# Kernel tuning notes

Measured on AMD Instinct MI355X. Metric: run time of the kernel, lower is better.

The kernel has to match this reference:

```python
import jax, jax.numpy as jnp
import numpy as np


def setup_inputs() -> dict:
    key = jax.random.key(0)
    k1, k2, k3 = jax.random.split(key, 3)
    B, A, C = 32, 16384, 81
    pred_logits = jax.random.normal(k1, (B, A, C), dtype=jnp.float32)
    target = jax.random.uniform(k2, (B, A, C), dtype=jnp.float32)
    depth = jax.random.randint(k3, (B, A, 1), 0, 3, dtype=jnp.int32)
    return {"pred_logits": pred_logits, "target": target, "depth": depth,
            "negpos_ratio": 3}


def reference(pred_logits, target, depth, negpos_ratio):
    B, A, C = pred_logits.shape
    # BCE-with-logits, elementwise (stable): softplus(x) - t*x
    ce = jax.nn.softplus(pred_logits) - target * pred_logits        # [B,A,C]
    max_ce = jnp.max(ce, axis=2)                                    # [B,A]
    depth_v = depth.reshape(B, A)
    # zero out rows already matched (positives) so they never rank as negatives
    max_ce = jnp.where(depth_v != 0, jnp.zeros((), ce.dtype), max_ce)
    # double-argsort rank trick: rank of each anchor in descending max_ce order
    order = jnp.argsort(-max_ce, axis=1)                            # [B,A]
    idx_rank = jnp.argsort(order, axis=1)                           # [B,A]
    num_pos = jnp.sum(depth_v > 0, axis=1)                          # [B]
    num_neg = jnp.minimum(negpos_ratio * num_pos, A - 1)            # [B]
    neg = idx_rank < num_neg[:, None]                               # [B,A] bool
    mask = (depth_v > 0) | neg                                      # [B,A] bool
    return ce * mask[:, :, None].astype(ce.dtype)                   # [B,A,C]
```

## Files before the change

kernel.cpp:

```cpp
#include <hip/hip_runtime.h>
#include <cstdint>
#include <cstddef>

#define NUM_C 81
#define NUM_A 16384
#define A_TILE 128
#define TILE_ELEMS (A_TILE * NUM_C)
#define TILE_F4    (TILE_ELEMS / 4)

__device__ __forceinline__ float ce_one(float x, float t) {
    float sp = fmaxf(x, 0.f) + __logf(1.f + __expf(-fabsf(x)));
    return fmaf(-t, x, sp);
}

__global__ __launch_bounds__(256)
void ce_max_tile(const float* __restrict__ logits,
                 const float* __restrict__ target,
                 const int* __restrict__ depth,
                 float* __restrict__ out,
                 float* __restrict__ max_ce,
                 int n_anchors) {
    __shared__ unsigned int smax[A_TILE];

    const int tid = threadIdx.x;
    if (tid < A_TILE) smax[tid] = 0u;
    __syncthreads();

    const int b = blockIdx.x;
    const size_t ebase = (size_t)b * TILE_ELEMS;
    const float4* lg4 = (const float4*)(logits + ebase);
    const float4* tg4 = (const float4*)(target + ebase);
    float4* o4 = (float4*)(out + ebase);

    for (int i = tid; i < TILE_F4; i += 256) {
        float4 x = lg4[i];
        float4 t = tg4[i];
        float4 c;
        c.x = ce_one(x.x, t.x);
        c.y = ce_one(x.y, t.y);
        c.z = ce_one(x.z, t.z);
        c.w = ce_one(x.w, t.w);
        o4[i] = c;

        const int e0 = 4 * i;
        const int a0 = e0 / NUM_C;
        const int r0 = e0 - a0 * NUM_C;
        if (r0 <= NUM_C - 4) {
            float m = fmaxf(fmaxf(c.x, c.y), fmaxf(c.z, c.w));
            atomicMax(&smax[a0], __float_as_uint(m));
        } else {
            const float vv[4] = {c.x, c.y, c.z, c.w};
            const int n0 = NUM_C - r0;
            float m0 = vv[0];
            for (int k = 1; k < n0; ++k) m0 = fmaxf(m0, vv[k]);
            float m1 = vv[n0];
            for (int k = n0 + 1; k < 4; ++k) m1 = fmaxf(m1, vv[k]);
            atomicMax(&smax[a0],     __float_as_uint(m0));
            atomicMax(&smax[a0 + 1], __float_as_uint(m1));
        }
    }
    __syncthreads();

    if (tid < A_TILE) {
        const int ga = b * A_TILE + tid;
        if (ga < n_anchors)
            max_ce[ga] = (depth[ga] != 0) ? 0.f : __uint_as_float(smax[tid]);
    }
}

__global__ __launch_bounds__(256)
void select_zero_kernel(const float* __restrict__ max_ce,
                        const int* __restrict__ depth,
                        const int* __restrict__ negpos_ratio,
                        float* __restrict__ out) {
    __shared__ unsigned int u[NUM_A];
    __shared__ int red[4];
    __shared__ int wave_eq[4];

    const int b   = blockIdx.x;
    const int tid = threadIdx.x;
    const int lane = tid & 63;
    const int wid  = tid >> 6;
    const float* mrow = max_ce + (size_t)b * NUM_A;
    const int*   drow = depth  + (size_t)b * NUM_A;
    uint4* u4 = (uint4*)u;

    auto phys = [](int i) -> int {
        return (i & ~15) | (((i & 15) + (i >> 4)) & 15);
    };

    const uint4* m4 = (const uint4*)mrow;
    const int4*  d4 = (const int4*)drow;
    int pos = 0;
    for (int i = tid; i < NUM_A / 4; i += 256) {
        uint4 v = m4[i];
        u4[phys(i)] = v;
        int4 dd = d4[i];
        pos += (dd.x > 0) + (dd.y > 0) + (dd.z > 0) + (dd.w > 0);
    }
    #pragma unroll
    for (int off = 32; off > 0; off >>= 1) pos += __shfl_down(pos, off, 64);
    if (lane == 0) red[wid] = pos;
    __syncthreads();
    const int num_pos = red[0] + red[1] + red[2] + red[3];

    int K = negpos_ratio[0] * num_pos;
    if (K > NUM_A - 1) K = NUM_A - 1;

    unsigned int T;
    int eq_quota;
    if (K <= 0) {
        T = 0xFFFFFFFFu;
        eq_quota = 0;
    } else {
        unsigned int p = 0;
        for (int bit = 31; bit >= 0; --bit) {
            unsigned int q = p | (1u << bit);
            int cnt = 0;
            #pragma unroll 4
            for (int j = 0; j < 16; ++j) {
                uint4 v = u4[16 * tid + ((j + tid) & 15)];
                cnt += (v.x >= q) + (v.y >= q) + (v.z >= q) + (v.w >= q);
            }
            #pragma unroll
            for (int off = 32; off > 0; off >>= 1) cnt += __shfl_down(cnt, off, 64);
            __syncthreads();
            if (lane == 0) red[wid] = cnt;
            __syncthreads();
            int total = red[0] + red[1] + red[2] + red[3];
            if (total >= K) p = q;
        }
        T = p;

        int gl = 0;
        #pragma unroll 4
        for (int j = 0; j < 16; ++j) {
            uint4 v = u4[16 * tid + ((j + tid) & 15)];
            gl += (v.x > T) + (v.y > T) + (v.z > T) + (v.w > T);
        }
        #pragma unroll
        for (int off = 32; off > 0; off >>= 1) gl += __shfl_down(gl, off, 64);
        __syncthreads();
        if (lane == 0) red[wid] = gl;
        __syncthreads();
        eq_quota = K - (red[0] + red[1] + red[2] + red[3]);
    }

    int eqc = 0;
    #pragma unroll 4
    for (int j = 0; j < 16; ++j) {
        uint4 v = u4[16 * tid + ((j + tid) & 15)];
        eqc += (v.x == T) + (v.y == T) + (v.z == T) + (v.w == T);
    }
    int inc = eqc;
    #pragma unroll
    for (int off = 1; off < 64; off <<= 1) {
        int n = __shfl_up(inc, off, 64);
        if (lane >= off) inc += n;
    }
    if (lane == 63) wave_eq[wid] = inc;
    __syncthreads();
    int woff = 0;
    for (int w = 0; w < wid; ++w) woff += wave_eq[w];
    int eqr = woff + (inc - eqc);

    float* orow = out + (size_t)b * NUM_A * NUM_C;
    const int base_a = tid * 64;
    for (int j = 0; j < 16; ++j) {
        uint4 v = u4[16 * tid + ((j + tid) & 15)];
        unsigned int vv[4] = {v.x, v.y, v.z, v.w};
        #pragma unroll
        for (int e = 0; e < 4; ++e) {
            int aa = base_a + 4 * j + e;
            unsigned int x = vv[e];
            bool selneg = (x > T);
            if (x == T) { selneg = (eqr < eq_quota); eqr++; }
            bool keep = (drow[aa] > 0) || selneg;
            if (!keep) {
                float* p = orow + (size_t)aa * NUM_C;
                #pragma unroll 9
                for (int c = 0; c < NUM_C; ++c) p[c] = 0.f;
            }
        }
    }
}

extern "C" void kernel_launch(void* const* d_in, const int* in_sizes, int n_in,
                              void* d_out, int out_size, void* d_ws, size_t ws_size,
                              hipStream_t stream) {
    const float* logits = (const float*)d_in[0];
    const float* target = (const float*)d_in[1];
    const int*   depth  = (const int*)d_in[2];
    const int*   negpos = (const int*)d_in[3];
    float* out = (float*)d_out;
    float* max_ce = (float*)d_ws;

    const int n_anchors = in_sizes[2];
    const int B = n_anchors / NUM_A;

    int blocks1 = (n_anchors + A_TILE - 1) / A_TILE;
    ce_max_tile<<<blocks1, 256, 0, stream>>>(logits, target, depth, out, max_ce, n_anchors);
    select_zero_kernel<<<B, 256, 0, stream>>>(max_ce, depth, negpos, out);
}
```

Baseline: 490.3 us.

## Software-pipeline CE tile loads, use nontemporal stores and occupancy hint

Restructures the CE/max tile loop so each thread prefetches the next two float4 pairs of logits and targets while computing the current two, with a tail for the remaining 32 float4s. Output stores become nontemporal, and launch bounds request 4 blocks per CU. The goal is to hide global load latency in this bandwidth-bound kernel and avoid polluting the cache with output. The cost is higher register pressure and a loop hardcoded to the tile size (2592 float4s).

```diff
diff --git a/kernel.cpp b/kernel.cpp
--- a/kernel.cpp
+++ b/kernel.cpp
@@ -8,12 +8,42 @@
 #define TILE_ELEMS (A_TILE * NUM_C)
 #define TILE_F4    (TILE_ELEMS / 4)
 
+typedef float f32x4 __attribute__((ext_vector_type(4)));
+
 __device__ __forceinline__ float ce_one(float x, float t) {
     float sp = fmaxf(x, 0.f) + __logf(1.f + __expf(-fabsf(x)));
     return fmaf(-t, x, sp);
 }
 
-__global__ __launch_bounds__(256)
+__device__ __forceinline__ void process4(int i, float4 x, float4 t,
+                                         f32x4* __restrict__ o4,
+                                         unsigned int* smax) {
+    f32x4 c;
+    c.x = ce_one(x.x, t.x);
+    c.y = ce_one(x.y, t.y);
+    c.z = ce_one(x.z, t.z);
+    c.w = ce_one(x.w, t.w);
+    __builtin_nontemporal_store(c, &o4[i]);
+
+    const int e0 = 4 * i;
+    const int a0 = e0 / NUM_C;
+    const int r0 = e0 - a0 * NUM_C;
+    if (r0 <= NUM_C - 4) {
+        float m = fmaxf(fmaxf(c.x, c.y), fmaxf(c.z, c.w));
+        atomicMax(&smax[a0], __float_as_uint(m));
+    } else {
+        const float vv[4] = {c.x, c.y, c.z, c.w};
+        const int n0 = NUM_C - r0;
+        float m0 = vv[0];
+        for (int k = 1; k < n0; ++k) m0 = fmaxf(m0, vv[k]);
+        float m1 = vv[n0];
+        for (int k = n0 + 1; k < 4; ++k) m1 = fmaxf(m1, vv[k]);
+        atomicMax(&smax[a0],     __float_as_uint(m0));
+        atomicMax(&smax[a0 + 1], __float_as_uint(m1));
+    }
+}
+
+__global__ __launch_bounds__(256, 4)
 void ce_max_tile(const float* __restrict__ logits,
                  const float* __restrict__ target,
                  const int* __restrict__ depth,
@@ -30,35 +60,28 @@
     const size_t ebase = (size_t)b * TILE_ELEMS;
     const float4* lg4 = (const float4*)(logits + ebase);
     const float4* tg4 = (const float4*)(target + ebase);
-    float4* o4 = (float4*)(out + ebase);
-
-    for (int i = tid; i < TILE_F4; i += 256) {
-        float4 x = lg4[i];
-        float4 t = tg4[i];
-        float4 c;
-        c.x = ce_one(x.x, t.x);
-        c.y = ce_one(x.y, t.y);
-        c.z = ce_one(x.z, t.z);
-        c.w = ce_one(x.w, t.w);
-        o4[i] = c;
-
-        const int e0 = 4 * i;
-        const int a0 = e0 / NUM_C;
-        const int r0 = e0 - a0 * NUM_C;
-        if (r0 <= NUM_C - 4) {
-            float m = fmaxf(fmaxf(c.x, c.y), fmaxf(c.z, c.w));
-            atomicMax(&smax[a0], __float_as_uint(m));
-        } else {
-            const float vv[4] = {c.x, c.y, c.z, c.w};
-            const int n0 = NUM_C - r0;
-            float m0 = vv[0];
-            for (int k = 1; k < n0; ++k) m0 = fmaxf(m0, vv[k]);
-            float m1 = vv[n0];
-            for (int k = n0 + 1; k < 4; ++k) m1 = fmaxf(m1, vv[k]);
-            atomicMax(&smax[a0],     __float_as_uint(m0));
-            atomicMax(&smax[a0 + 1], __float_as_uint(m1));
-        }
-    }
+    f32x4* o4 = (f32x4*)(out + ebase);
+
+    int i = tid;
+    float4 xa = lg4[i],       ta = tg4[i];
+    float4 xb = lg4[i + 256], tb = tg4[i + 256];
+
+    for (int j = 0; j < 5; ++j) {
+        const int inext = i + 512;
+        float4 xc, tc, xd, td;
+        if (j < 4) {
+            xc = lg4[inext];       tc = tg4[inext];
+            xd = lg4[inext + 256]; td = tg4[inext + 256];
+        } else if (tid < 32) {
+            xc = lg4[2560 + tid];  tc = tg4[2560 + tid];
+        }
+        process4(i,       xa, ta, o4, smax);
+        process4(i + 256, xb, tb, o4, smax);
+        i = inext;
+        xa = xc; ta = tc; xb = xd; tb = td;
+    }
+    if (tid < 32) process4(2560 + tid, xa, ta, o4, smax);
+
     __syncthreads();
 
     if (tid < A_TILE) {
```

Result: no change. 496.7 us (+1.3%).
